# Kernel tuning notes

Measured on AMD Instinct MI355X. Metric: run time of the kernel, lower is better.

The kernel has to match this reference:

```python
import jax, jax.numpy as jnp
import numpy as np

H = 128          # hidden_dim
EPS = 1e-5       # BatchNorm eps


def _mean_aggr(h_src, src_idx, dst_idx, num_dst):
    # scatter-mean of h_src rows (gathered by src_idx) onto dst nodes
    msgs = h_src[src_idx]                                   # [E, H] gather
    s = jax.ops.segment_sum(msgs, dst_idx, num_segments=num_dst)
    c = jax.ops.segment_sum(jnp.ones((dst_idx.shape[0],), h_src.dtype),
                            dst_idx, num_segments=num_dst)
    return s / jnp.maximum(c, 1.0)[:, None]


def _bn_eval(h, g, b, m, v):
    return (h - m) * jax.lax.rsqrt(v + EPS) * g + b


def setup_inputs() -> dict:
    key = jax.random.key(0)
    ks = jax.random.split(key, 32)
    Nu, Nr, E, Din, ED = 100000, 100000, 500000, 32, 16
    d = {}
    d['x_user'] = jax.random.normal(ks[0], (Nu, Din), jnp.float32)
    d['x_recipient'] = jax.random.normal(ks[1], (Nr, Din), jnp.float32)
    d['edge_attr'] = jax.random.normal(ks[2], (E, ED), jnp.float32)
    d['edge_index_ut'] = jax.random.randint(ks[3], (2, E), 0, Nr)  # user->recipient
    d['edge_index_ru'] = jax.random.randint(ks[4], (2, E), 0, Nu)  # recipient->user
    sc = 0.05
    # input projections (Linear: y = x @ W + b, W stored [in, out])
    d['proj_uW'] = jax.random.normal(ks[5], (Din, H), jnp.float32) * sc
    d['proj_ub'] = jnp.zeros((H,), jnp.float32)
    d['proj_rW'] = jax.random.normal(ks[6], (Din, H), jnp.float32) * sc
    d['proj_rb'] = jnp.zeros((H,), jnp.float32)
    # SAGEConv params: [num_layers=2, num_edge_types=2, ...]
    d['sage_Wl'] = jax.random.normal(ks[7], (2, 2, H, H), jnp.float32) * sc
    d['sage_bl'] = jnp.zeros((2, 2, H), jnp.float32)
    d['sage_Wr'] = jax.random.normal(ks[8], (2, 2, H, H), jnp.float32) * sc
    # BatchNorm (eval): [num_layers=2, num_node_types=2 (0=user,1=recipient), H]
    d['bn_g'] = jnp.ones((2, 2, H), jnp.float32)
    d['bn_b'] = jnp.zeros((2, 2, H), jnp.float32)
    d['bn_m'] = jax.random.normal(ks[9], (2, 2, H), jnp.float32) * 0.01
    d['bn_v'] = jnp.ones((2, 2, H), jnp.float32)
    # EdgePredictor MLP: (2H + edge_dim) -> H -> H//2 -> 1
    din = 2 * H + ED
    d['ep_W1'] = jax.random.normal(ks[10], (din, H), jnp.float32) * sc
    d['ep_b1'] = jnp.zeros((H,), jnp.float32)
    d['ep_bng'] = jnp.ones((H,), jnp.float32)
    d['ep_bnb'] = jnp.zeros((H,), jnp.float32)
    d['ep_bnm'] = jax.random.normal(ks[11], (H,), jnp.float32) * 0.01
    d['ep_bnv'] = jnp.ones((H,), jnp.float32)
    d['ep_W2'] = jax.random.normal(ks[12], (H, H // 2), jnp.float32) * sc
    d['ep_b2'] = jnp.zeros((H // 2,), jnp.float32)
    d['ep_W3'] = jax.random.normal(ks[13], (H // 2, 1), jnp.float32) * sc
    d['ep_b3'] = jnp.zeros((1,), jnp.float32)
    return d


def reference(x_user, x_recipient, edge_attr, edge_index_ut, edge_index_ru,
              proj_uW, proj_ub, proj_rW, proj_rb,
              sage_Wl, sage_bl, sage_Wr,
              bn_g, bn_b, bn_m, bn_v,
              ep_W1, ep_b1, ep_bng, ep_bnb, ep_bnm, ep_bnv,
              ep_W2, ep_b2, ep_W3, ep_b3):
    Nu = x_user.shape[0]
    Nr = x_recipient.shape[0]
    # input projections
    h_u = x_user @ proj_uW + proj_ub        # [Nu, H]
    h_r = x_recipient @ proj_rW + proj_rb   # [Nr, H]

    for i in range(2):  # num_layers
        # edge type 0: user -> recipient (SAGE mean aggr + root)
        agg_r = _mean_aggr(h_u, edge_index_ut[0], edge_index_ut[1], Nr)
        new_r = agg_r @ sage_Wl[i, 0] + sage_bl[i, 0] + h_r @ sage_Wr[i, 0]
        # edge type 1: recipient -> user
        agg_u = _mean_aggr(h_r, edge_index_ru[0], edge_index_ru[1], Nu)
        new_u = agg_u @ sage_Wl[i, 1] + sage_bl[i, 1] + h_u @ sage_Wr[i, 1]
        # BN (eval) + ReLU (dropout inactive) + residual
        new_u = jax.nn.relu(_bn_eval(new_u, bn_g[i, 0], bn_b[i, 0], bn_m[i, 0], bn_v[i, 0])) + h_u
        new_r = jax.nn.relu(_bn_eval(new_r, bn_g[i, 1], bn_b[i, 1], bn_m[i, 1], bn_v[i, 1])) + h_r
        h_u, h_r = new_u, new_r

    # edge predictor on target edge type (user -> recipient)
    src = h_u[edge_index_ut[0]]   # [E, H]
    dst = h_r[edge_index_ut[1]]   # [E, H]
    x = jnp.concatenate([src, dst, edge_attr], axis=1)  # [E, 2H+ED]
    h = jax.nn.relu(x @ ep_W1 + ep_b1)
    h = _bn_eval(h, ep_bng, ep_bnb, ep_bnm, ep_bnv)
    h = jax.nn.relu(h @ ep_W2 + ep_b2)
    out = jax.nn.sigmoid(h @ ep_W3 + ep_b3)
    return out.squeeze(-1)  # [E]
```

## Files before the change

### kernel.cpp

```cpp
#include <hip/hip_runtime.h>
#include <math.h>

#define H 128
#define BN_EPS 1e-5f

typedef __attribute__((ext_vector_type(8))) short bf16x8;
typedef __attribute__((ext_vector_type(4))) float f32x4;

__device__ __forceinline__ unsigned short f2bf(float f) {
    unsigned int u = __float_as_uint(f);
    u += 0x7fffu + ((u >> 16) & 1u);
    return (unsigned short)(u >> 16);
}
__device__ __forceinline__ float bf2f(unsigned short s) {
    return __uint_as_float(((unsigned int)s) << 16);
}
__device__ __forceinline__ f32x4 mfma16(bf16x8 a, bf16x8 b, f32x4 c) {
    return __builtin_amdgcn_mfma_f32_16x16x32_bf16(a, b, c, 0, 0, 0);
}

__device__ __forceinline__ void wfrag_one(const float* __restrict__ src,
                                          unsigned short* __restrict__ dst,
                                          int K, int N, int idx) {
    int l = idx & 63;
    int rest = idx >> 6;
    int ntn = N >> 4;
    int nt = rest % ntn;
    int kc = rest / ntn;
    int n = nt * 16 + (l & 15);
    int k0 = kc * 32 + (l >> 4) * 8;
    bf16x8 v;
    #pragma unroll
    for (int j = 0; j < 8; ++j) {
        int k = k0 + j;
        v[j] = (short)((k < K) ? f2bf(src[(size_t)k * N + n]) : 0);
    }
    *(bf16x8*)(dst + (size_t)idx * 8) = v;
}

__global__ __launch_bounds__(256)
void wfrag_all(const float* __restrict__ W1, const float* __restrict__ W2,
               const float* __restrict__ pu, const float* __restrict__ pr,
               const float* __restrict__ Wl, const float* __restrict__ Wr,
               unsigned short* __restrict__ W1f, unsigned short* __restrict__ W2f,
               unsigned short* __restrict__ puf, unsigned short* __restrict__ prf,
               unsigned short* __restrict__ sageWf) {
    int bx = blockIdx.x;
    if (bx < 26) {
        int idx = bx * 256 + threadIdx.x;
        if (idx < 4608)      wfrag_one(W1, W1f, 272, 128, idx);
        else if (idx < 5632) wfrag_one(W2, W2f, 128, 64, idx - 4608);
        else if (idx < 6144) wfrag_one(pu, puf, 32, 128, idx - 5632);
        else if (idx < 6656) wfrag_one(pr, prf, 32, 128, idx - 6144);
    } else {
        int idx = (bx - 26) * 256 + threadIdx.x;
        int seg = idx >> 11;
        int sub = idx & 2047;
        int lt = seg >> 1;
        int half = seg & 1;
        const float* src = (half ? Wr : Wl) + (size_t)lt * H * H;
        unsigned short* dst = sageWf + (size_t)lt * 32768 + half * 16384;
        wfrag_one(src, dst, 128, 128, sub);
    }
}

__global__ __launch_bounds__(256)
void proj_kernel(const float* __restrict__ xu, const float* __restrict__ xr,
                 const unsigned short* __restrict__ puf, const float* __restrict__ bu,
                 const unsigned short* __restrict__ prf, const float* __restrict__ br,
                 unsigned short* __restrict__ hub, unsigned short* __restrict__ hrb,
                 int Nu, int Nr, int nbu) {
    int bx = blockIdx.x;
    const float* x; const unsigned short* Wf; const float* bias;
    unsigned short* hb; int N; int row0;
    if (bx < nbu) { x = xu; Wf = puf; bias = bu; hb = hub; N = Nu; row0 = bx * 64; }
    else          { x = xr; Wf = prf; bias = br; hb = hrb; N = Nr; row0 = (bx - nbu) * 64; }

    int tid = threadIdx.x, l = tid & 63, w = tid >> 6, l15 = l & 15, quad = l >> 4;
    int arow = row0 + w * 16 + l15;

    bf16x8 a = {0, 0, 0, 0, 0, 0, 0, 0};
    if (arow < N) {
        const float* xp = x + (size_t)arow * 32 + quad * 8;
        float4 v0 = *(const float4*)xp;
        float4 v1 = *(const float4*)(xp + 4);
        a[0] = (short)f2bf(v0.x); a[1] = (short)f2bf(v0.y);
        a[2] = (short)f2bf(v0.z); a[3] = (short)f2bf(v0.w);
        a[4] = (short)f2bf(v1.x); a[5] = (short)f2bf(v1.y);
        a[6] = (short)f2bf(v1.z); a[7] = (short)f2bf(v1.w);
    }
    f32x4 acc[8];
    #pragma unroll
    for (int nt = 0; nt < 8; ++nt) {
        bf16x8 b = *(const bf16x8*)(Wf + (size_t)(nt * 64 + l) * 8);
        acc[nt] = mfma16(a, b, (f32x4){0.f, 0.f, 0.f, 0.f});
    }
    #pragma unroll
    for (int reg = 0; reg < 4; ++reg) {
        int row = row0 + w * 16 + quad * 4 + reg;
        if (row < N) {
            #pragma unroll
            for (int nt = 0; nt < 8; ++nt) {
                int col = nt * 16 + l15;
                hb[(size_t)row * H + col] = f2bf(acc[nt][reg] + bias[col]);
            }
        }
    }
}

__global__ __launch_bounds__(256)
void hist_kernel(const int* __restrict__ dstR, const int* __restrict__ dstU,
                 int* __restrict__ degR, int* __restrict__ degU, int E, int EB) {
    int bx = blockIdx.x;
    const int* dst = (bx < EB) ? dstR : dstU;
    int* deg = (bx < EB) ? degR : degU;
    int e = ((bx < EB) ? bx : bx - EB) * 256 + threadIdx.x;
    if (e < E) atomicAdd(&deg[dst[e]], 1);
}

__global__ __launch_bounds__(256)
void scan1_kernel(const int* __restrict__ degR, const int* __restrict__ degU,
                  int* __restrict__ partR, int* __restrict__ partU, int Nr, int Nu, int NBr) {
    int bx = blockIdx.x;
    const int* deg = (bx < NBr) ? degR : degU;
    int* part = (bx < NBr) ? partR : partU;
    int lb = (bx < NBr) ? bx : bx - NBr;
    int N = (bx < NBr) ? Nr : Nu;
    __shared__ int s[256];
    int t = threadIdx.x;
    int i = lb * 256 + t;
    s[t] = (i < N) ? deg[i] : 0;
    __syncthreads();
    for (int o = 128; o > 0; o >>= 1) {
        if (t < o) s[t] += s[t + o];
        __syncthreads();
    }
    if (t == 0) part[lb] = s[0];
}

__global__ __launch_bounds__(512)
void scan2_kernel(int* __restrict__ partR, int* __restrict__ partU, int nbR, int nbU) {
    int* part = (blockIdx.x == 0) ? partR : partU;
    int nb = (blockIdx.x == 0) ? nbR : nbU;
    __shared__ int s[512];
    int t = threadIdx.x;
    int v = (t < nb) ? part[t] : 0;
    s[t] = v;
    __syncthreads();
    for (int o = 1; o < 512; o <<= 1) {
        int x = (t >= o) ? s[t - o] : 0;
        __syncthreads();
        s[t] += x;
        __syncthreads();
    }
    if (t < nb) part[t] = s[t] - v;
}

__global__ __launch_bounds__(256)
void scan3_kernel(const int* __restrict__ degR, const int* __restrict__ degU,
                  const int* __restrict__ partR, const int* __restrict__ partU,
                  int* __restrict__ offR, int* __restrict__ offU, int Nr, int Nu, int NBr) {
    int bx = blockIdx.x;
    const int* deg = (bx < NBr) ? degR : degU;
    const int* part = (bx < NBr) ? partR : partU;
    int* off = (bx < NBr) ? offR : offU;
    int lb = (bx < NBr) ? bx : bx - NBr;
    int N = (bx < NBr) ? Nr : Nu;
    __shared__ int s[256];
    int t = threadIdx.x;
    int i = lb * 256 + t;
    int v = (i < N) ? deg[i] : 0;
    s[t] = v;
    __syncthreads();
    for (int o = 1; o < 256; o <<= 1) {
        int x = (t >= o) ? s[t - o] : 0;
        __syncthreads();
        s[t] += x;
        __syncthreads();
    }
    if (i < N) off[i] = part[lb] + s[t] - v;
    if (i == N - 1) off[N] = part[lb] + s[t];
}

__global__ __launch_bounds__(256)
void fill_kernel(const int* __restrict__ srcR, const int* __restrict__ dstR,
                 const int* __restrict__ srcU, const int* __restrict__ dstU,
                 const int* __restrict__ offR, const int* __restrict__ offU,
                 int* __restrict__ degR, int* __restrict__ degU,
                 int* __restrict__ eidR, int* __restrict__ eidU, int E, int EB) {
    int bx = blockIdx.x;
    const int* src = (bx < EB) ? srcR : srcU;
    const int* dst = (bx < EB) ? dstR : dstU;
    const int* off = (bx < EB) ? offR : offU;
    int* deg = (bx < EB) ? degR : degU;
    int* eid = (bx < EB) ? eidR : eidU;
    int e = ((bx < EB) ? bx : bx - EB) * 256 + threadIdx.x;
    if (e < E) {
        int d = dst[e];
        int p = off[d] + atomicSub(&deg[d], 1) - 1;
        eid[p] = src[e];
    }
}

__global__ __launch_bounds__(256)
void layer_kernel(const unsigned short* __restrict__ hu_o, const unsigned short* __restrict__ hr_o,
                  unsigned short* __restrict__ hu_n, unsigned short* __restrict__ hr_n,
                  const int* __restrict__ off_r, const int* __restrict__ eid_r,
                  const int* __restrict__ off_u, const int* __restrict__ eid_u,
                  int Nu, int Nr, int nbr,
                  const unsigned short* __restrict__ WfR, const float* __restrict__ blR,
                  const float* __restrict__ gR, const float* __restrict__ bR,
                  const float* __restrict__ mR, const float* __restrict__ vR,
                  const unsigned short* __restrict__ WfU, const float* __restrict__ blU,
                  const float* __restrict__ gU, const float* __restrict__ bU,
                  const float* __restrict__ mU, const float* __restrict__ vU) {
    int bx = blockIdx.x;
    const unsigned short* gsrc; const unsigned short* own; unsigned short* outp;
    const int* off; const int* eid; const unsigned short* Wf;
    const float *bl, *bg, *bb, *bm, *bv;
    int N, row0;
    if (bx < nbr) {
        gsrc = hu_o; own = hr_o; outp = hr_n; off = off_r; eid = eid_r;
        Wf = WfR; bl = blR; bg = gR; bb = bR; bm = mR; bv = vR;
        N = Nr; row0 = bx * 64;
    } else {
        gsrc = hr_o; own = hu_o; outp = hu_n; off = off_u; eid = eid_u;
        Wf = WfU; bl = blU; bg = gU; bb = bU; bm = mU; bv = vU;
        N = Nu; row0 = (bx - nbr) * 64;
    }

    __shared__ float sc[128], sh[128], bias[128];
    int tid = threadIdx.x;
    if (tid < 128) {
        float s = bg[tid] * rsqrtf(bv[tid] + BN_EPS);
        sc[tid] = s;
        sh[tid] = bb[tid] - bm[tid] * s;
        bias[tid] = bl[tid];
    }
    __syncthreads();

    int l = tid & 63, w = tid >> 6, l15 = l & 15, quad = l >> 4;
    int arow = row0 + w * 16 + l15;
    bool rok = (arow < N);
    size_t rbase = (size_t)(rok ? arow : 0) * H;
    int s0 = rok ? off[arow] : 0;
    int s1 = rok ? off[arow + 1] : 0;

    float ag[4][8];
    #pragma unroll
    for (int kc = 0; kc < 4; ++kc)
        #pragma unroll
        for (int j = 0; j < 8; ++j) ag[kc][j] = 0.0f;

    for (int i = s0; i < s1; ++i) {
        int s = eid[i];
        const unsigned short* rp = gsrc + (size_t)s * H + quad * 8;
        #pragma unroll
        for (int kc = 0; kc < 4; ++kc) {
            bf16x8 v = *(const bf16x8*)(rp + kc * 32);
            #pragma unroll
            for (int j = 0; j < 8; ++j) ag[kc][j] += bf2f((unsigned short)v[j]);
        }
    }
    float inv = (s1 > s0) ? 1.0f / (float)(s1 - s0) : 0.0f;

    f32x4 acc[8];
    #pragma unroll
    for (int nt = 0; nt < 8; ++nt) acc[nt] = (f32x4){0.f, 0.f, 0.f, 0.f};

    #pragma unroll
    for (int kc = 0; kc < 4; ++kc) {
        bf16x8 a;
        #pragma unroll
        for (int j = 0; j < 8; ++j) a[j] = (short)f2bf(ag[kc][j] * inv);
        #pragma unroll
        for (int nt = 0; nt < 8; ++nt) {
            bf16x8 b = *(const bf16x8*)(Wf + (size_t)((kc * 8 + nt) * 64 + l) * 8);
            acc[nt] = mfma16(a, b, acc[nt]);
        }
    }
    #pragma unroll
    for (int kc = 4; kc < 8; ++kc) {
        bf16x8 a = *(const bf16x8*)(own + rbase + (kc - 4) * 32 + quad * 8);
        #pragma unroll
        for (int nt = 0; nt < 8; ++nt) {
            bf16x8 b = *(const bf16x8*)(Wf + (size_t)((kc * 8 + nt) * 64 + l) * 8);
            acc[nt] = mfma16(a, b, acc[nt]);
        }
    }

    #pragma unroll
    for (int reg = 0; reg < 4; ++reg) {
        int crow = row0 + w * 16 + quad * 4 + reg;
        if (crow < N) {
            #pragma unroll
            for (int nt = 0; nt < 8; ++nt) {
                int col = nt * 16 + l15;
                float g = acc[nt][reg] + bias[col];
                g = g * sc[col] + sh[col];
                float hv = bf2f(own[(size_t)crow * H + col]);
                outp[(size_t)crow * H + col] = f2bf(fmaxf(g, 0.0f) + hv);
            }
        }
    }
}

__global__ __launch_bounds__(256)
void ep_kernel(const unsigned short* __restrict__ hub, const unsigned short* __restrict__ hrb,
               const float* __restrict__ ea, const int* __restrict__ esrc,
               const int* __restrict__ edst,
               const unsigned short* __restrict__ W1f, const float* __restrict__ b1,
               const float* __restrict__ bng, const float* __restrict__ bnb,
               const float* __restrict__ bnm, const float* __restrict__ bnv,
               const unsigned short* __restrict__ W2f, const float* __restrict__ b2,
               const float* __restrict__ W3, const float* __restrict__ b3,
               float* __restrict__ out, int E) {
    __shared__ unsigned short h1s[64][136];
    __shared__ int se[64], de[64];
    __shared__ float sc1[128], sh1[128], bi1[128];

    int tid = threadIdx.x;
    int e0 = blockIdx.x * 64;
    if (tid < 64) {
        int e = e0 + tid;
        se[tid] = (e < E) ? esrc[e] : 0;
        de[tid] = (e < E) ? edst[e] : 0;
    }
    if (tid < 128) {
        float s = bng[tid] * rsqrtf(bnv[tid] + BN_EPS);
        sc1[tid] = s;
        sh1[tid] = bnb[tid] - bnm[tid] * s;
        bi1[tid] = b1[tid];
    }
    __syncthreads();

    int l = tid & 63, w = tid >> 6, l15 = l & 15, quad = l >> 4;
    int arow = w * 16 + l15;
    size_t soff = (size_t)se[arow] * H;
    size_t doff = (size_t)de[arow] * H;
    int e = e0 + arow;
    bool ev = (e < E);

    f32x4 acc[8];
    #pragma unroll
    for (int nt = 0; nt < 8; ++nt) acc[nt] = (f32x4){0.f, 0.f, 0.f, 0.f};

    #pragma unroll
    for (int kc = 0; kc < 9; ++kc) {
        bf16x8 a;
        if (kc < 4) {
            a = *(const bf16x8*)(hub + soff + kc * 32 + quad * 8);
        } else if (kc < 8) {
            a = *(const bf16x8*)(hrb + doff + (kc - 4) * 32 + quad * 8);
        } else {
            a = (bf16x8){0, 0, 0, 0, 0, 0, 0, 0};
            if (quad < 2 && ev) {
                const float* p = ea + (size_t)e * 16 + quad * 8;
                float4 v0 = *(const float4*)p;
                float4 v1 = *(const float4*)(p + 4);
                a[0] = (short)f2bf(v0.x); a[1] = (short)f2bf(v0.y);
                a[2] = (short)f2bf(v0.z); a[3] = (short)f2bf(v0.w);
                a[4] = (short)f2bf(v1.x); a[5] = (short)f2bf(v1.y);
                a[6] = (short)f2bf(v1.z); a[7] = (short)f2bf(v1.w);
            }
        }
        #pragma unroll
        for (int nt = 0; nt < 8; ++nt) {
            bf16x8 b = *(const bf16x8*)(W1f + (size_t)((kc * 8 + nt) * 64 + l) * 8);
            acc[nt] = mfma16(a, b, acc[nt]);
        }
    }

    #pragma unroll
    for (int nt = 0; nt < 8; ++nt) {
        #pragma unroll
        for (int reg = 0; reg < 4; ++reg) {
            int row = w * 16 + quad * 4 + reg;
            int col = nt * 16 + l15;
            float z = acc[nt][reg] + bi1[col];
            z = fmaxf(z, 0.0f);
            z = z * sc1[col] + sh1[col];
            h1s[row][col] = f2bf(z);
        }
    }
    __syncthreads();

    f32x4 acc2[4];
    #pragma unroll
    for (int nt = 0; nt < 4; ++nt) acc2[nt] = (f32x4){0.f, 0.f, 0.f, 0.f};
    #pragma unroll
    for (int kc = 0; kc < 4; ++kc) {
        bf16x8 a2 = *(const bf16x8*)&h1s[w * 16 + l15][kc * 32 + quad * 8];
        #pragma unroll
        for (int nt = 0; nt < 4; ++nt) {
            bf16x8 b = *(const bf16x8*)(W2f + (size_t)((kc * 4 + nt) * 64 + l) * 8);
            acc2[nt] = mfma16(a2, b, acc2[nt]);
        }
    }

    float part[4] = {0.f, 0.f, 0.f, 0.f};
    #pragma unroll
    for (int nt = 0; nt < 4; ++nt) {
        int col = nt * 16 + l15;
        float w3v = W3[col];
        float b2v = b2[col];
        #pragma unroll
        for (int reg = 0; reg < 4; ++reg)
            part[reg] += fmaxf(acc2[nt][reg] + b2v, 0.0f) * w3v;
    }
    #pragma unroll
    for (int m = 1; m < 16; m <<= 1) {
        #pragma unroll
        for (int reg = 0; reg < 4; ++reg)
            part[reg] += __shfl_xor(part[reg], m);
    }
    if (l15 < 4) {
        int row = w * 16 + quad * 4 + l15;
        int ee = e0 + row;
        if (ee < E) out[ee] = 1.0f / (1.0f + expf(-(part[l15] + b3[0])));
    }
}

extern "C" void kernel_launch(void* const* d_in, const int* in_sizes, int n_in,
                              void* d_out, int out_size, void* d_ws, size_t ws_size,
                              hipStream_t stream) {
    const float* x_u     = (const float*)d_in[0];
    const float* x_r     = (const float*)d_in[1];
    const float* eattr   = (const float*)d_in[2];
    const int*   ei_ut   = (const int*)d_in[3];
    const int*   ei_ru   = (const int*)d_in[4];
    const float* proj_uW = (const float*)d_in[5];
    const float* proj_ub = (const float*)d_in[6];
    const float* proj_rW = (const float*)d_in[7];
    const float* proj_rb = (const float*)d_in[8];
    const float* sage_Wl = (const float*)d_in[9];
    const float* sage_bl = (const float*)d_in[10];
    const float* sage_Wr = (const float*)d_in[11];
    const float* bn_g    = (const float*)d_in[12];
    const float* bn_b    = (const float*)d_in[13];
    const float* bn_m    = (const float*)d_in[14];
    const float* bn_v    = (const float*)d_in[15];
    const float* ep_W1   = (const float*)d_in[16];
    const float* ep_b1   = (const float*)d_in[17];
    const float* ep_bng  = (const float*)d_in[18];
    const float* ep_bnb  = (const float*)d_in[19];
    const float* ep_bnm  = (const float*)d_in[20];
    const float* ep_bnv  = (const float*)d_in[21];
    const float* ep_W2   = (const float*)d_in[22];
    const float* ep_b2   = (const float*)d_in[23];
    const float* ep_W3   = (const float*)d_in[24];
    const float* ep_b3   = (const float*)d_in[25];

    int Nu = in_sizes[0] / 32;
    int Nr = in_sizes[1] / 32;
    int E  = in_sizes[3] / 2;

    unsigned short* us = (unsigned short*)d_ws;
    unsigned short* h0_u = us;   us += (size_t)Nu * H;
    unsigned short* h0_r = us;   us += (size_t)Nr * H;
    unsigned short* h1_u = us;   us += (size_t)Nu * H;
    unsigned short* h1_r = us;   us += (size_t)Nr * H;
    unsigned short* W1f  = us;   us += 36864;
    unsigned short* W2f  = us;   us += 8192;
    unsigned short* puf  = us;   us += 4096;
    unsigned short* prf  = us;   us += 4096;
    unsigned short* sageWf = us; us += 131072;
    int* ip    = (int*)us;
    int* off_r = ip;  ip += Nr + 1;
    int* off_u = ip;  ip += Nu + 1;
    int* deg_r = ip;  ip += Nr;
    int* deg_u = ip;  ip += Nu;
    int* eid_r = ip;  ip += E;
    int* eid_u = ip;  ip += E;
    int* part_r = ip; ip += 512;
    int* part_u = ip; ip += 512;

    const int* ut_src = ei_ut;
    const int* ut_dst = ei_ut + E;
    const int* ru_src = ei_ru;
    const int* ru_dst = ei_ru + E;

    int EB  = (E + 255) / 256;
    int NBr = (Nr + 255) / 256;
    int NBu = (Nu + 255) / 256;

    wfrag_all<<<90, 256, 0, stream>>>(ep_W1, ep_W2, proj_uW, proj_rW,
                                      sage_Wl, sage_Wr,
                                      W1f, W2f, puf, prf, sageWf);

    hipMemsetAsync(deg_r, 0, (size_t)(Nr + Nu) * sizeof(int), stream);
    hist_kernel<<<2 * EB, 256, 0, stream>>>(ut_dst, ru_dst, deg_r, deg_u, E, EB);
    scan1_kernel<<<NBr + NBu, 256, 0, stream>>>(deg_r, deg_u, part_r, part_u, Nr, Nu, NBr);
    scan2_kernel<<<2, 512, 0, stream>>>(part_r, part_u, NBr, NBu);
    scan3_kernel<<<NBr + NBu, 256, 0, stream>>>(deg_r, deg_u, part_r, part_u,
                                                off_r, off_u, Nr, Nu, NBr);
    fill_kernel<<<2 * EB, 256, 0, stream>>>(ut_src, ut_dst, ru_src, ru_dst,
                                            off_r, off_u, deg_r, deg_u,
                                            eid_r, eid_u, E, EB);

    int nbu = (Nu + 63) / 64, nbr = (Nr + 63) / 64;
    proj_kernel<<<nbu + nbr, 256, 0, stream>>>(x_u, x_r, puf, proj_ub, prf, proj_rb,
                                               h0_u, h0_r, Nu, Nr, nbu);

    for (int layer = 0; layer < 2; ++layer) {
        const unsigned short* iu = (layer == 0) ? h0_u : h1_u;
        const unsigned short* ir = (layer == 0) ? h0_r : h1_r;
        unsigned short* ou = (layer == 0) ? h1_u : h0_u;
        unsigned short* orr = (layer == 0) ? h1_r : h0_r;

        const unsigned short* Wf0 = sageWf + ((size_t)layer * 2 + 0) * 32768;
        const unsigned short* Wf1 = sageWf + ((size_t)layer * 2 + 1) * 32768;
        const float* bl0 = sage_bl + ((size_t)layer * 2 + 0) * H;
        const float* bl1 = sage_bl + ((size_t)layer * 2 + 1) * H;
        const float* g0 = bn_g + ((size_t)layer * 2 + 0) * H;
        const float* b0 = bn_b + ((size_t)layer * 2 + 0) * H;
        const float* m0 = bn_m + ((size_t)layer * 2 + 0) * H;
        const float* v0 = bn_v + ((size_t)layer * 2 + 0) * H;
        const float* g1 = bn_g + ((size_t)layer * 2 + 1) * H;
        const float* b1 = bn_b + ((size_t)layer * 2 + 1) * H;
        const float* m1 = bn_m + ((size_t)layer * 2 + 1) * H;
        const float* v1 = bn_v + ((size_t)layer * 2 + 1) * H;

        layer_kernel<<<nbr + nbu, 256, 0, stream>>>(
            iu, ir, ou, orr,
            off_r, eid_r, off_u, eid_u,
            Nu, Nr, nbr,
            Wf0, bl0, g1, b1, m1, v1,
            Wf1, bl1, g0, b0, m0, v0);
    }

    ep_kernel<<<(E + 63) / 64, 256, 0, stream>>>(h0_u, h0_r, eattr, ut_src, ut_dst,
                                                 W1f, ep_b1,
                                                 ep_bng, ep_bnb, ep_bnm, ep_bnv,
                                                 W2f, ep_b2, ep_W3, ep_b3,
                                                 (float*)d_out, E);
}
```

Before: 567.3 us.

## Bucket nodes by degree for layer kernel and process edges in CSR order

Adds a degree-bucketing pass (histogram, scan, scatter) that permutes node rows so each 64-row block of the layer kernel holds nodes of similar in-degree. This is meant to reduce lane divergence in the per-row gather loop. The edge predictor now walks edges in destination-sorted CSR order, using saved permutation and destination arrays, so that dst-row gathers are more local. The cost is three extra small kernels, extra index arrays, scattered output and edge_attr accesses through the permutation, and non-contiguous row writes in the layer kernel.

```diff
diff --git a/kernel.cpp b/kernel.cpp
--- a/kernel.cpp
+++ b/kernel.cpp
@@ -187,18 +187,77 @@
                  const int* __restrict__ srcU, const int* __restrict__ dstU,
                  const int* __restrict__ offR, const int* __restrict__ offU,
                  int* __restrict__ degR, int* __restrict__ degU,
-                 int* __restrict__ eidR, int* __restrict__ eidU, int E, int EB) {
-    int bx = blockIdx.x;
-    const int* src = (bx < EB) ? srcR : srcU;
-    const int* dst = (bx < EB) ? dstR : dstU;
-    const int* off = (bx < EB) ? offR : offU;
-    int* deg = (bx < EB) ? degR : degU;
-    int* eid = (bx < EB) ? eidR : eidU;
-    int e = ((bx < EB) ? bx : bx - EB) * 256 + threadIdx.x;
+                 int* __restrict__ eidR, int* __restrict__ eidU,
+                 int* __restrict__ epermR, int* __restrict__ epdstR,
+                 int E, int EB) {
+    int bx = blockIdx.x;
+    bool isR = bx < EB;
+    const int* src = isR ? srcR : srcU;
+    const int* dst = isR ? dstR : dstU;
+    const int* off = isR ? offR : offU;
+    int* deg = isR ? degR : degU;
+    int* eid = isR ? eidR : eidU;
+    int e = (isR ? bx : bx - EB) * 256 + threadIdx.x;
     if (e < E) {
         int d = dst[e];
         int p = off[d] + atomicSub(&deg[d], 1) - 1;
         eid[p] = src[e];
+        if (isR) {
+            epermR[p] = e;
+            epdstR[p] = d;
+        }
+    }
+}
+
+__global__ __launch_bounds__(256)
+void dhist_kernel(const int* __restrict__ off_r, const int* __restrict__ off_u,
+                  int* __restrict__ bhist, int Nr, int Nu, int NBr) {
+    int bx = blockIdx.x;
+    bool isR = bx < NBr;
+    const int* off = isR ? off_r : off_u;
+    int* bh = bhist + (isR ? 0 : 64);
+    int N = isR ? Nr : Nu;
+    int n = (isR ? bx : bx - NBr) * 256 + threadIdx.x;
+    if (n < N) {
+        int d = off[n + 1] - off[n];
+        atomicAdd(&bh[min(d, 63)], 1);
+    }
+}
+
+__global__ __launch_bounds__(64)
+void dscan_kernel(const int* __restrict__ bhist, int* __restrict__ boff) {
+    __shared__ int s[64];
+    int t = threadIdx.x;
+    int base = blockIdx.x * 64;
+    int v = bhist[base + t];
+    s[t] = v;
+    __syncthreads();
+    for (int o = 1; o < 64; o <<= 1) {
+        int x = (t >= o) ? s[t - o] : 0;
+        __syncthreads();
+        s[t] += x;
+        __syncthreads();
+    }
+    boff[base + t] = s[t] - v;
+}
+
+__global__ __launch_bounds__(256)
+void dscatter_kernel(const int* __restrict__ off_r, const int* __restrict__ off_u,
+                     const int* __restrict__ boff, int* __restrict__ bcnt,
+                     int* __restrict__ npr, int* __restrict__ npu,
+                     int Nr, int Nu, int NBr) {
+    int bx = blockIdx.x;
+    bool isR = bx < NBr;
+    const int* off = isR ? off_r : off_u;
+    const int* bo = boff + (isR ? 0 : 64);
+    int* bc = bcnt + (isR ? 0 : 64);
+    int* np = isR ? npr : npu;
+    int N = isR ? Nr : Nu;
+    int n = (isR ? bx : bx - NBr) * 256 + threadIdx.x;
+    if (n < N) {
+        int b = min(off[n + 1] - off[n], 63);
+        int pos = bo[b] + atomicAdd(&bc[b], 1);
+        np[pos] = n;
     }
 }
 
@@ -207,6 +266,7 @@
                   unsigned short* __restrict__ hu_n, unsigned short* __restrict__ hr_n,
                   const int* __restrict__ off_r, const int* __restrict__ eid_r,
                   const int* __restrict__ off_u, const int* __restrict__ eid_u,
+                  const int* __restrict__ np_r, const int* __restrict__ np_u,
                   int Nu, int Nr, int nbr,
                   const unsigned short* __restrict__ WfR, const float* __restrict__ blR,
                   const float* __restrict__ gR, const float* __restrict__ bR,
@@ -216,20 +276,21 @@
                   const float* __restrict__ mU, const float* __restrict__ vU) {
     int bx = blockIdx.x;
     const unsigned short* gsrc; const unsigned short* own; unsigned short* outp;
-    const int* off; const int* eid; const unsigned short* Wf;
+    const int* off; const int* eid; const int* np; const unsigned short* Wf;
     const float *bl, *bg, *bb, *bm, *bv;
     int N, row0;
     if (bx < nbr) {
-        gsrc = hu_o; own = hr_o; outp = hr_n; off = off_r; eid = eid_r;
+        gsrc = hu_o; own = hr_o; outp = hr_n; off = off_r; eid = eid_r; np = np_r;
         Wf = WfR; bl = blR; bg = gR; bb = bR; bm = mR; bv = vR;
         N = Nr; row0 = bx * 64;
     } else {
-        gsrc = hr_o; own = hu_o; outp = hu_n; off = off_u; eid = eid_u;
+        gsrc = hr_o; own = hu_o; outp = hu_n; off = off_u; eid = eid_u; np = np_u;
         Wf = WfU; bl = blU; bg = gU; bb = bU; bm = mU; bv = vU;
         N = Nu; row0 = (bx - nbr) * 64;
     }
 
     __shared__ float sc[128], sh[128], bias[128];
+    __shared__ int pidx[64];
     int tid = threadIdx.x;
     if (tid < 128) {
         float s = bg[tid] * rsqrtf(bv[tid] + BN_EPS);
@@ -237,14 +298,19 @@
         sh[tid] = bb[tid] - bm[tid] * s;
         bias[tid] = bl[tid];
     }
+    if (tid < 64) {
+        int rr = row0 + tid;
+        pidx[tid] = (rr < N) ? np[rr] : -1;
+    }
     __syncthreads();
 
     int l = tid & 63, w = tid >> 6, l15 = l & 15, quad = l >> 4;
-    int arow = row0 + w * 16 + l15;
-    bool rok = (arow < N);
-    size_t rbase = (size_t)(rok ? arow : 0) * H;
-    int s0 = rok ? off[arow] : 0;
-    int s1 = rok ? off[arow + 1] : 0;
+    int rb = w * 16 + l15;
+    int phys = pidx[rb];
+    bool rok = (phys >= 0);
+    size_t rbase = (size_t)(rok ? phys : 0) * H;
+    int s0 = rok ? off[phys] : 0;
+    int s1 = rok ? off[phys + 1] : 0;
 
     float ag[4][8];
     #pragma unroll
@@ -281,7 +347,8 @@
     }
     #pragma unroll
     for (int kc = 4; kc < 8; ++kc) {
-        bf16x8 a = *(const bf16x8*)(own + rbase + (kc - 4) * 32 + quad * 8);
+        bf16x8 a = rok ? *(const bf16x8*)(own + rbase + (kc - 4) * 32 + quad * 8)
+                       : (bf16x8){0, 0, 0, 0, 0, 0, 0, 0};
         #pragma unroll
         for (int nt = 0; nt < 8; ++nt) {
             bf16x8 b = *(const bf16x8*)(Wf + (size_t)((kc * 8 + nt) * 64 + l) * 8);
@@ -291,15 +358,16 @@
 
     #pragma unroll
     for (int reg = 0; reg < 4; ++reg) {
-        int crow = row0 + w * 16 + quad * 4 + reg;
-        if (crow < N) {
+        int crb = w * 16 + quad * 4 + reg;
+        int cphys = pidx[crb];
+        if (cphys >= 0) {
             #pragma unroll
             for (int nt = 0; nt < 8; ++nt) {
                 int col = nt * 16 + l15;
                 float g = acc[nt][reg] + bias[col];
                 g = g * sc[col] + sh[col];
-                float hv = bf2f(own[(size_t)crow * H + col]);
-                outp[(size_t)crow * H + col] = f2bf(fmaxf(g, 0.0f) + hv);
+                float hv = bf2f(own[(size_t)cphys * H + col]);
+                outp[(size_t)cphys * H + col] = f2bf(fmaxf(g, 0.0f) + hv);
             }
         }
     }
@@ -307,8 +375,9 @@
 
 __global__ __launch_bounds__(256)
 void ep_kernel(const unsigned short* __restrict__ hub, const unsigned short* __restrict__ hrb,
-               const float* __restrict__ ea, const int* __restrict__ esrc,
-               const int* __restrict__ edst,
+               const float* __restrict__ ea,
+               const int* __restrict__ slot_src, const int* __restrict__ slot_dst,
+               const int* __restrict__ slot_eid,
                const unsigned short* __restrict__ W1f, const float* __restrict__ b1,
                const float* __restrict__ bng, const float* __restrict__ bnb,
                const float* __restrict__ bnm, const float* __restrict__ bnv,
@@ -316,15 +385,17 @@
                const float* __restrict__ W3, const float* __restrict__ b3,
                float* __restrict__ out, int E) {
     __shared__ unsigned short h1s[64][136];
-    __shared__ int se[64], de[64];
+    __shared__ int se[64], de[64], pe[64];
     __shared__ float sc1[128], sh1[128], bi1[128];
 
     int tid = threadIdx.x;
-    int e0 = blockIdx.x * 64;
+    int p0 = blockIdx.x * 64;
     if (tid < 64) {
-        int e = e0 + tid;
-        se[tid] = (e < E) ? esrc[e] : 0;
-        de[tid] = (e < E) ? edst[e] : 0;
+        int p = p0 + tid;
+        bool v = (p < E);
+        se[tid] = v ? slot_src[p] : 0;
+        de[tid] = v ? slot_dst[p] : 0;
+        pe[tid] = v ? slot_eid[p] : 0;
     }
     if (tid < 128) {
         float s = bng[tid] * rsqrtf(bnv[tid] + BN_EPS);
@@ -338,8 +409,8 @@
     int arow = w * 16 + l15;
     size_t soff = (size_t)se[arow] * H;
     size_t doff = (size_t)de[arow] * H;
-    int e = e0 + arow;
-    bool ev = (e < E);
+    int eorig = pe[arow];
+    bool ev = (p0 + arow < E);
 
     f32x4 acc[8];
     #pragma unroll
@@ -355,7 +426,7 @@
         } else {
             a = (bf16x8){0, 0, 0, 0, 0, 0, 0, 0};
             if (quad < 2 && ev) {
-                const float* p = ea + (size_t)e * 16 + quad * 8;
+                const float* p = ea + (size_t)eorig * 16 + quad * 8;
                 float4 v0 = *(const float4*)p;
                 float4 v1 = *(const float4*)(p + 4);
                 a[0] = (short)f2bf(v0.x); a[1] = (short)f2bf(v0.y);
@@ -416,8 +487,10 @@
     }
     if (l15 < 4) {
         int row = w * 16 + quad * 4 + l15;
-        int ee = e0 + row;
-        if (ee < E) out[ee] = 1.0f / (1.0f + expf(-(part[l15] + b3[0])));
+        if (p0 + row < E) {
+            int eo = pe[row];
+            out[eo] = 1.0f / (1.0f + expf(-(part[l15] + b3[0])));
+        }
     }
 }
 
@@ -465,15 +538,22 @@
     unsigned short* puf  = us;   us += 4096;
     unsigned short* prf  = us;   us += 4096;
     unsigned short* sageWf = us; us += 131072;
-    int* ip    = (int*)us;
-    int* off_r = ip;  ip += Nr + 1;
-    int* off_u = ip;  ip += Nu + 1;
-    int* deg_r = ip;  ip += Nr;
-    int* deg_u = ip;  ip += Nu;
-    int* eid_r = ip;  ip += E;
-    int* eid_u = ip;  ip += E;
-    int* part_r = ip; ip += 512;
-    int* part_u = ip; ip += 512;
+    int* ip     = (int*)us;
+    int* off_r  = ip;  ip += Nr + 1;
+    int* off_u  = ip;  ip += Nu + 1;
+    int* deg_r  = ip;  ip += Nr;
+    int* deg_u  = ip;  ip += Nu;
+    int* bhist  = ip;  ip += 128;
+    int* bcnt   = ip;  ip += 128;
+    int* boff   = ip;  ip += 128;
+    int* eid_r  = ip;  ip += E;
+    int* eid_u  = ip;  ip += E;
+    int* eperm_r = ip; ip += E;
+    int* epdst_r = ip; ip += E;
+    int* np_r   = ip;  ip += Nr;
+    int* np_u   = ip;  ip += Nu;
+    int* part_r = ip;  ip += 512;
+    int* part_u = ip;  ip += 512;
 
     const int* ut_src = ei_ut;
     const int* ut_dst = ei_ut + E;
@@ -488,7 +568,7 @@
                                       sage_Wl, sage_Wr,
                                       W1f, W2f, puf, prf, sageWf);
 
-    hipMemsetAsync(deg_r, 0, (size_t)(Nr + Nu) * sizeof(int), stream);
+    hipMemsetAsync(deg_r, 0, (size_t)(Nr + Nu + 256) * sizeof(int), stream);
     hist_kernel<<<2 * EB, 256, 0, stream>>>(ut_dst, ru_dst, deg_r, deg_u, E, EB);
     scan1_kernel<<<NBr + NBu, 256, 0, stream>>>(deg_r, deg_u, part_r, part_u, Nr, Nu, NBr);
     scan2_kernel<<<2, 512, 0, stream>>>(part_r, part_u, NBr, NBu);
@@ -496,7 +576,11 @@
                                                 off_r, off_u, Nr, Nu, NBr);
     fill_kernel<<<2 * EB, 256, 0, stream>>>(ut_src, ut_dst, ru_src, ru_dst,
                                             off_r, off_u, deg_r, deg_u,
-                                            eid_r, eid_u, E, EB);
+                                            eid_r, eid_u, eperm_r, epdst_r, E, EB);
+    dhist_kernel<<<NBr + NBu, 256, 0, stream>>>(off_r, off_u, bhist, Nr, Nu, NBr);
+    dscan_kernel<<<2, 64, 0, stream>>>(bhist, boff);
+    dscatter_kernel<<<NBr + NBu, 256, 0, stream>>>(off_r, off_u, boff, bcnt,
+                                                   np_r, np_u, Nr, Nu, NBr);
 
     int nbu = (Nu + 63) / 64, nbr = (Nr + 63) / 64;
     proj_kernel<<<nbu + nbr, 256, 0, stream>>>(x_u, x_r, puf, proj_ub, prf, proj_rb,
@@ -523,13 +607,14 @@
 
         layer_kernel<<<nbr + nbu, 256, 0, stream>>>(
             iu, ir, ou, orr,
-            off_r, eid_r, off_u, eid_u,
+            off_r, eid_r, off_u, eid_u, np_r, np_u,
             Nu, Nr, nbr,
             Wf0, bl0, g1, b1, m1, v1,
             Wf1, bl1, g0, b0, m0, v0);
     }
 
-    ep_kernel<<<(E + 63) / 64, 256, 0, stream>>>(h0_u, h0_r, eattr, ut_src, ut_dst,
+    ep_kernel<<<(E + 63) / 64, 256, 0, stream>>>(h0_u, h0_r, eattr,
+                                                 eid_r, epdst_r, eperm_r,
                                                  W1f, ep_b1,
                                                  ep_bng, ep_bnb, ep_bnm, ep_bnv,
                                                  W2f, ep_b2, ep_W3, ep_b3,
```

Measured after the change: 1.601 ms. 182% more time.

## Process edge predictor in destination-sorted order and prefetch A fragments

Applied to the files above, without the earlier changes.

The fill kernel now records, for each CSR slot of the user->recipient graph, the original edge id and the destination node. The edge predictor iterates over edges in that destination-sorted order, so consecutive edges share recipient rows and gathers of h_r hit cache more often, and it scatters outputs back to their original edge ids. It also hoists all A-fragment loads (in the edge predictor and the SAGE layer's own-row fragments) ahead of the MFMA loops so the global loads overlap. In exchange it writes two extra E-sized index arrays, adds scattered edge_attr reads and output writes, and raises register pressure from holding the prefetched fragments.

```diff
diff --git a/kernel.cpp b/kernel.cpp
--- a/kernel.cpp
+++ b/kernel.cpp
@@ -187,18 +187,25 @@
                  const int* __restrict__ srcU, const int* __restrict__ dstU,
                  const int* __restrict__ offR, const int* __restrict__ offU,
                  int* __restrict__ degR, int* __restrict__ degU,
-                 int* __restrict__ eidR, int* __restrict__ eidU, int E, int EB) {
-    int bx = blockIdx.x;
-    const int* src = (bx < EB) ? srcR : srcU;
-    const int* dst = (bx < EB) ? dstR : dstU;
-    const int* off = (bx < EB) ? offR : offU;
-    int* deg = (bx < EB) ? degR : degU;
-    int* eid = (bx < EB) ? eidR : eidU;
-    int e = ((bx < EB) ? bx : bx - EB) * 256 + threadIdx.x;
+                 int* __restrict__ eidR, int* __restrict__ eidU,
+                 int* __restrict__ epermR, int* __restrict__ epdstR,
+                 int E, int EB) {
+    int bx = blockIdx.x;
+    bool isR = bx < EB;
+    const int* src = isR ? srcR : srcU;
+    const int* dst = isR ? dstR : dstU;
+    const int* off = isR ? offR : offU;
+    int* deg = isR ? degR : degU;
+    int* eid = isR ? eidR : eidU;
+    int e = (isR ? bx : bx - EB) * 256 + threadIdx.x;
     if (e < E) {
         int d = dst[e];
         int p = off[d] + atomicSub(&deg[d], 1) - 1;
         eid[p] = src[e];
+        if (isR) {
+            epermR[p] = e;
+            epdstR[p] = d;
+        }
     }
 }
 
@@ -246,6 +253,11 @@
     int s0 = rok ? off[arow] : 0;
     int s1 = rok ? off[arow + 1] : 0;
 
+    bf16x8 ownfr[4];
+    #pragma unroll
+    for (int kc = 0; kc < 4; ++kc)
+        ownfr[kc] = *(const bf16x8*)(own + rbase + kc * 32 + quad * 8);
+
     float ag[4][8];
     #pragma unroll
     for (int kc = 0; kc < 4; ++kc)
@@ -281,11 +293,10 @@
     }
     #pragma unroll
     for (int kc = 4; kc < 8; ++kc) {
-        bf16x8 a = *(const bf16x8*)(own + rbase + (kc - 4) * 32 + quad * 8);
         #pragma unroll
         for (int nt = 0; nt < 8; ++nt) {
             bf16x8 b = *(const bf16x8*)(Wf + (size_t)((kc * 8 + nt) * 64 + l) * 8);
-            acc[nt] = mfma16(a, b, acc[nt]);
+            acc[nt] = mfma16(ownfr[kc - 4], b, acc[nt]);
         }
     }
 
@@ -307,8 +318,9 @@
 
 __global__ __launch_bounds__(256)
 void ep_kernel(const unsigned short* __restrict__ hub, const unsigned short* __restrict__ hrb,
-               const float* __restrict__ ea, const int* __restrict__ esrc,
-               const int* __restrict__ edst,
+               const float* __restrict__ ea,
+               const int* __restrict__ slot_src, const int* __restrict__ slot_dst,
+               const int* __restrict__ slot_eid,
                const unsigned short* __restrict__ W1f, const float* __restrict__ b1,
                const float* __restrict__ bng, const float* __restrict__ bnb,
                const float* __restrict__ bnm, const float* __restrict__ bnv,
@@ -316,15 +328,17 @@
                const float* __restrict__ W3, const float* __restrict__ b3,
                float* __restrict__ out, int E) {
     __shared__ unsigned short h1s[64][136];
-    __shared__ int se[64], de[64];
+    __shared__ int se[64], de[64], pe[64];
     __shared__ float sc1[128], sh1[128], bi1[128];
 
     int tid = threadIdx.x;
-    int e0 = blockIdx.x * 64;
+    int p0 = blockIdx.x * 64;
     if (tid < 64) {
-        int e = e0 + tid;
-        se[tid] = (e < E) ? esrc[e] : 0;
-        de[tid] = (e < E) ? edst[e] : 0;
+        int p = p0 + tid;
+        bool v = (p < E);
+        se[tid] = v ? slot_src[p] : 0;
+        de[tid] = v ? slot_dst[p] : 0;
+        pe[tid] = v ? slot_eid[p] : 0;
     }
     if (tid < 128) {
         float s = bng[tid] * rsqrtf(bnv[tid] + BN_EPS);
@@ -338,8 +352,29 @@
     int arow = w * 16 + l15;
     size_t soff = (size_t)se[arow] * H;
     size_t doff = (size_t)de[arow] * H;
-    int e = e0 + arow;
-    bool ev = (e < E);
+    int eorig = pe[arow];
+    bool ev = (p0 + arow < E);
+
+    bf16x8 afr[9];
+    #pragma unroll
+    for (int kc = 0; kc < 4; ++kc)
+        afr[kc] = *(const bf16x8*)(hub + soff + kc * 32 + quad * 8);
+    #pragma unroll
+    for (int kc = 0; kc < 4; ++kc)
+        afr[4 + kc] = *(const bf16x8*)(hrb + doff + kc * 32 + quad * 8);
+    {
+        bf16x8 a = {0, 0, 0, 0, 0, 0, 0, 0};
+        if (quad < 2 && ev) {
+            const float* p = ea + (size_t)eorig * 16 + quad * 8;
+            float4 v0 = *(const float4*)p;
+            float4 v1 = *(const float4*)(p + 4);
+            a[0] = (short)f2bf(v0.x); a[1] = (short)f2bf(v0.y);
+            a[2] = (short)f2bf(v0.z); a[3] = (short)f2bf(v0.w);
+            a[4] = (short)f2bf(v1.x); a[5] = (short)f2bf(v1.y);
+            a[6] = (short)f2bf(v1.z); a[7] = (short)f2bf(v1.w);
+        }
+        afr[8] = a;
+    }
 
     f32x4 acc[8];
     #pragma unroll
@@ -347,27 +382,10 @@
 
     #pragma unroll
     for (int kc = 0; kc < 9; ++kc) {
-        bf16x8 a;
-        if (kc < 4) {
-            a = *(const bf16x8*)(hub + soff + kc * 32 + quad * 8);
-        } else if (kc < 8) {
-            a = *(const bf16x8*)(hrb + doff + (kc - 4) * 32 + quad * 8);
-        } else {
-            a = (bf16x8){0, 0, 0, 0, 0, 0, 0, 0};
-            if (quad < 2 && ev) {
-                const float* p = ea + (size_t)e * 16 + quad * 8;
-                float4 v0 = *(const float4*)p;
-                float4 v1 = *(const float4*)(p + 4);
-                a[0] = (short)f2bf(v0.x); a[1] = (short)f2bf(v0.y);
-                a[2] = (short)f2bf(v0.z); a[3] = (short)f2bf(v0.w);
-                a[4] = (short)f2bf(v1.x); a[5] = (short)f2bf(v1.y);
-                a[6] = (short)f2bf(v1.z); a[7] = (short)f2bf(v1.w);
-            }
-        }
         #pragma unroll
         for (int nt = 0; nt < 8; ++nt) {
             bf16x8 b = *(const bf16x8*)(W1f + (size_t)((kc * 8 + nt) * 64 + l) * 8);
-            acc[nt] = mfma16(a, b, acc[nt]);
+            acc[nt] = mfma16(afr[kc], b, acc[nt]);
         }
     }
 
@@ -416,8 +434,10 @@
     }
     if (l15 < 4) {
         int row = w * 16 + quad * 4 + l15;
-        int ee = e0 + row;
-        if (ee < E) out[ee] = 1.0f / (1.0f + expf(-(part[l15] + b3[0])));
+        if (p0 + row < E) {
+            int eo = pe[row];
+            out[eo] = 1.0f / (1.0f + expf(-(part[l15] + b3[0])));
+        }
     }
 }
 
@@ -465,15 +485,17 @@
     unsigned short* puf  = us;   us += 4096;
     unsigned short* prf  = us;   us += 4096;
     unsigned short* sageWf = us; us += 131072;
-    int* ip    = (int*)us;
-    int* off_r = ip;  ip += Nr + 1;
-    int* off_u = ip;  ip += Nu + 1;
-    int* deg_r = ip;  ip += Nr;
-    int* deg_u = ip;  ip += Nu;
-    int* eid_r = ip;  ip += E;
-    int* eid_u = ip;  ip += E;
-    int* part_r = ip; ip += 512;
-    int* part_u = ip; ip += 512;
+    int* ip     = (int*)us;
+    int* off_r  = ip;  ip += Nr + 1;
+    int* off_u  = ip;  ip += Nu + 1;
+    int* deg_r  = ip;  ip += Nr;
+    int* deg_u  = ip;  ip += Nu;
+    int* eid_r  = ip;  ip += E;
+    int* eid_u  = ip;  ip += E;
+    int* eperm_r = ip; ip += E;
+    int* epdst_r = ip; ip += E;
+    int* part_r = ip;  ip += 512;
+    int* part_u = ip;  ip += 512;
 
     const int* ut_src = ei_ut;
     const int* ut_dst = ei_ut + E;
@@ -496,7 +518,7 @@
                                                 off_r, off_u, Nr, Nu, NBr);
     fill_kernel<<<2 * EB, 256, 0, stream>>>(ut_src, ut_dst, ru_src, ru_dst,
                                             off_r, off_u, deg_r, deg_u,
-                                            eid_r, eid_u, E, EB);
+                                            eid_r, eid_u, eperm_r, epdst_r, E, EB);
 
     int nbu = (Nu + 63) / 64, nbr = (Nr + 63) / 64;
     proj_kernel<<<nbu + nbr, 256, 0, stream>>>(x_u, x_r, puf, proj_ub, prf, proj_rb,
@@ -529,7 +551,8 @@
             Wf1, bl1, g0, b0, m0, v0);
     }
 
-    ep_kernel<<<(E + 63) / 64, 256, 0, stream>>>(h0_u, h0_r, eattr, ut_src, ut_dst,
+    ep_kernel<<<(E + 63) / 64, 256, 0, stream>>>(h0_u, h0_r, eattr,
+                                                 eid_r, epdst_r, eperm_r,
                                                  W1f, ep_b1,
                                                  ep_bng, ep_bnb, ep_bnm, ep_bnv,
                                                  W2f, ep_b2, ep_W3, ep_b3,
```

New measurement: 578.8 us. 2.0% more time.
